# Performance work log

Measured on AMD Instinct MI355X. Metric: run time of the kernel, lower is better.

The kernel has to match this reference:

```python
import jax, jax.numpy as jnp
import numpy as np

N, E = 50000, 640000
IN, HD, OUT, NCLS = 768, 128, 128, 2
H, C = 4, 32  # heads, per-head channels (HD/H = OUT/H = 32)
NEG_SLOPE = 0.2


def _glorot(key, shape):
    fan_in, fan_out = shape[0], shape[1]
    lim = jnp.sqrt(6.0 / (fan_in + fan_out))
    return jax.random.uniform(key, shape, jnp.float32, -lim, lim)


def setup_inputs() -> dict:
    key = jax.random.key(0)
    ks = jax.random.split(key, 24)
    x = jax.random.normal(ks[0], (1, N, IN), jnp.float32)
    edge_index = jax.random.randint(ks[1], (2, E), 0, N, jnp.int64)
    d = {"x": x, "edge_index": edge_index}
    ins = [IN, HD, HD, HD]
    for i in range(4):
        d[f"Wl{i+1}"] = _glorot(ks[2 + 5 * i], (ins[i], H * C))
        d[f"Wr{i+1}"] = _glorot(ks[3 + 5 * i], (ins[i], H * C))
        d[f"att{i+1}"] = _glorot(ks[4 + 5 * i], (H, C))
        d[f"b{i+1}"] = jnp.zeros((H * C,), jnp.float32)
    d["clfW"] = _glorot(ks[22], (OUT, NCLS))
    d["clfb"] = jnp.zeros((NCLS,), jnp.float32)
    return d


def _gatv2_layer(x, Wl, Wr, att, b, src, dst):
    # x: [N, F_in] -> out: [N, H*C]. GATv2: e = a^T LeakyReLU(xl_j + xr_i)
    xl = (x @ Wl).reshape(N, H, C)
    xr = (x @ Wr).reshape(N, H, C)
    h = xl[src] + xr[dst]                                   # [E', H, C] per-edge gather
    e = jnp.einsum('ehc,hc->eh', jax.nn.leaky_relu(h, NEG_SLOPE), att)
    m = jax.ops.segment_max(e, dst, num_segments=N)          # scatter-softmax (stable)
    a = jnp.exp(e - m[dst])
    s = jax.ops.segment_sum(a, dst, num_segments=N)
    alpha = a / (s[dst] + 1e-16)
    out = jax.ops.segment_sum(alpha[..., None] * xl[src], dst, num_segments=N)
    return out.reshape(N, H * C) + b


def reference(x, edge_index, Wl1, Wr1, att1, b1, Wl2, Wr2, att2, b2,
              Wl3, Wr3, att3, b3, Wl4, Wr4, att4, b4, clfW, clfb):
    xn = x.reshape(N, IN)  # torch.squeeze
    loops = jnp.arange(N, dtype=edge_index.dtype)  # PyG add_self_loops=True
    src = jnp.concatenate([edge_index[0], loops])
    dst = jnp.concatenate([edge_index[1], loops])
    h = jax.nn.relu(_gatv2_layer(xn, Wl1, Wr1, att1, b1, src, dst))
    h = jax.nn.relu(_gatv2_layer(h, Wl2, Wr2, att2, b2, src, dst))
    h = jax.nn.relu(_gatv2_layer(h, Wl3, Wr3, att3, b3, src, dst))
    h = _gatv2_layer(h, Wl4, Wr4, att4, b4, src, dst)        # [N, OUT]
    g = jnp.mean(h, axis=0, keepdims=True)                   # unsqueeze+mean over nodes -> [1, OUT]
    return g @ clfW + clfb                                   # [1, NCLS]
```

## Files before the change

### kernel.cpp

```cpp
#include <hip/hip_runtime.h>
#include <hip/hip_bf16.h>
#include <hip/hip_fp16.h>

#define NN 50000
#define EE 640000
#define HC 128
#define NB1 196

typedef _Float16 f16x8 __attribute__((ext_vector_type(8)));
typedef _Float16 h2 __attribute__((ext_vector_type(2)));
typedef float f32x4 __attribute__((ext_vector_type(4)));
typedef unsigned short u16;

__device__ __forceinline__ u16 f2h(float f) {
    return __builtin_bit_cast(u16, (_Float16)f);
}
__device__ __forceinline__ h2 bch2(unsigned a) { return __builtin_bit_cast(h2, a); }
__device__ __forceinline__ h2 habs2(h2 a) {
    return __builtin_bit_cast(h2, __builtin_bit_cast(unsigned, a) & 0x7FFF7FFFu);
}

__device__ __forceinline__ void gload_lds16(const void* g, void* l) {
    __builtin_amdgcn_global_load_lds((const __attribute__((address_space(1))) void*)g,
                                     (__attribute__((address_space(3))) void*)l, 16, 0, 0);
}

__device__ __forceinline__ float red8(float x) {
    x += __int_as_float(__builtin_amdgcn_update_dpp(0, __float_as_int(x), 0xB1, 0xF, 0xF, true));
    x += __int_as_float(__builtin_amdgcn_update_dpp(0, __float_as_int(x), 0x4E, 0xF, 0xF, true));
    x += __int_as_float(__builtin_amdgcn_ds_swizzle(__float_as_int(x), 0x101F));
    return x;
}


__global__ void k_count(const int* __restrict__ ei, int* __restrict__ cnt) {
    int e = blockIdx.x * blockDim.x + threadIdx.x;
    if (e < EE) atomicAdd(&cnt[ei[EE + e]], 1);
}

__global__ void k_bsum(const int* __restrict__ cnt, int* __restrict__ bsum) {
    __shared__ int sd[256];
    int b = blockIdx.x, t = threadIdx.x, i = b * 256 + t;
    sd[t] = (i < NN) ? cnt[i] + 1 : 0;
    __syncthreads();
    for (int o = 128; o; o >>= 1) { if (t < o) sd[t] += sd[t + o]; __syncthreads(); }
    if (!t) bsum[b] = sd[0];
}

__global__ void k_offs(const int* __restrict__ cnt_in, const int* __restrict__ bsum,
                       int* __restrict__ offs, int* __restrict__ cursor,
                       int* __restrict__ csr) {
    __shared__ int sb[256];
    __shared__ int sd[256];
    int b = blockIdx.x, t = threadIdx.x, i = b * 256 + t;
    sb[t] = (t < NB1) ? bsum[t] : 0;
    int v = (i < NN) ? cnt_in[i] + 1 : 0;
    sd[t] = v;
    __syncthreads();
    for (int o = 1; o < 256; o <<= 1) {
        int u1 = (t >= o) ? sd[t - o] : 0;
        int u2 = (t >= o) ? sb[t - o] : 0;
        __syncthreads();
        sd[t] += u1; sb[t] += u2;
        __syncthreads();
    }
    int bex = (b > 0) ? sb[b - 1] : 0;
    if (i < NN) {
        int o = bex + sd[t] - v;
        offs[i] = o;
        csr[o] = i;
        cursor[i] = o + 1;
    }
    if (b == NB1 - 1 && t == 0) offs[NN] = sb[NB1 - 1];
}

__global__ void k_fill(const int* __restrict__ ei, int* __restrict__ cursor,
                       int* __restrict__ csr) {
    int e = blockIdx.x * blockDim.x + threadIdx.x;
    if (e < EE) {
        int s = ei[e], d = ei[EE + e];
        int pos = atomicAdd(&cursor[d], 1);
        csr[pos] = s;
    }
}


#define WT_L0 196608
#define WT_LX 32768
#define WT_TOT (WT_L0 + 3 * WT_LX)

__global__ void k_castw_all(const float* __restrict__ Wl1, const float* __restrict__ Wr1,
                            const float* __restrict__ Wl2, const float* __restrict__ Wr2,
                            const float* __restrict__ Wl3, const float* __restrict__ Wr3,
                            const float* __restrict__ Wl4, const float* __restrict__ Wr4,
                            u16* __restrict__ WtAll) {
    int gid = blockIdx.x * 256 + threadIdx.x;
    if (gid >= WT_TOT) return;
    const float *Wl, *Wr;
    int idx, K, base;
    if (gid < WT_L0) { Wl = Wl1; Wr = Wr1; idx = gid; K = 768; base = 0; }
    else {
        int r = gid - WT_L0;
        int l = r >> 15; idx = r & (WT_LX - 1); K = 128; base = WT_L0 + l * WT_LX;
        if (l == 0)      { Wl = Wl2; Wr = Wr2; }
        else if (l == 1) { Wl = Wl3; Wr = Wr3; }
        else             { Wl = Wl4; Wr = Wr4; }
    }
    int c = idx / K, k = idx - c * K;
    float v = (c < 128) ? Wl[k * 128 + c] : Wr[k * 128 + (c - 128)];
    WtAll[base + idx] = f2h(v);
}


template<int K, bool F32A>
__global__ __launch_bounds__(512, 4)
void k_gemm(const void* __restrict__ Ag, const u16* __restrict__ Wt,
            u16* __restrict__ xb) {
    __shared__ __align__(16) u16 As[128 * 64];
    __shared__ __align__(16) u16 Bs[256 * 64];
    const int tid = threadIdx.x;
    const int wv = tid >> 6, ln = tid & 63;
    const int wr = wv >> 2, wc = wv & 3;
    const int m0 = blockIdx.x * 128;
    const int lrow = ln & 15, g = ln >> 4;

    f32x4 acc[4][4] = {};

    const float* Af = (const float*)Ag;
    const u16* Ab = (const u16*)Ag;
    const int arow = tid >> 2, aq = tid & 3;
    int arg = m0 + arow; if (arg >= NN) arg = 0;
    float4 ra0, ra1, ra2, ra3;

    if constexpr (F32A) {
        const float* src = Af + (size_t)arg * K + aq * 16;
        ra0 = *(const float4*)(src);
        ra1 = *(const float4*)(src + 4);
        ra2 = *(const float4*)(src + 8);
        ra3 = *(const float4*)(src + 12);
    }

    constexpr int NSTEP = K / 64;
    for (int ks = 0; ks < NSTEP; ++ks) {
        if constexpr (F32A) {
            const int s = arow & 7;
            f16x8 v0, v1;
            v0[0] = (_Float16)ra0.x; v0[1] = (_Float16)ra0.y;
            v0[2] = (_Float16)ra0.z; v0[3] = (_Float16)ra0.w;
            v0[4] = (_Float16)ra1.x; v0[5] = (_Float16)ra1.y;
            v0[6] = (_Float16)ra1.z; v0[7] = (_Float16)ra1.w;
            v1[0] = (_Float16)ra2.x; v1[1] = (_Float16)ra2.y;
            v1[2] = (_Float16)ra2.z; v1[3] = (_Float16)ra2.w;
            v1[4] = (_Float16)ra3.x; v1[5] = (_Float16)ra3.y;
            v1[6] = (_Float16)ra3.z; v1[7] = (_Float16)ra3.w;
            *(f16x8*)&As[arow * 64 + (((aq * 2) ^ s) * 8)] = v0;
            *(f16x8*)&As[arow * 64 + (((aq * 2 + 1) ^ s) * 8)] = v1;
        } else {
            #pragma unroll
            for (int q = 0; q < 2; ++q) {
                int r8 = (wv * 2 + q) * 8;
                int row = r8 + (ln >> 3);
                int lc = (ln & 7) ^ (row & 7);
                int rg = m0 + row; if (rg >= NN) rg = 0;
                gload_lds16(Ab + (size_t)rg * K + ks * 64 + lc * 8, &As[r8 * 64]);
            }
        }
        #pragma unroll
        for (int q = 0; q < 4; ++q) {
            int r8 = (wv * 4 + q) * 8;
            int row = r8 + (ln >> 3);
            int lc = (ln & 7) ^ (row & 7);
            gload_lds16(Wt + (size_t)row * K + ks * 64 + lc * 8, &Bs[r8 * 64]);
        }
        __syncthreads();

        if constexpr (F32A) {
            if (ks + 1 < NSTEP) {
                const float* src = Af + (size_t)arg * K + (ks + 1) * 64 + aq * 16;
                ra0 = *(const float4*)(src);
                ra1 = *(const float4*)(src + 4);
                ra2 = *(const float4*)(src + 8);
                ra3 = *(const float4*)(src + 12);
            }
        }

        #pragma unroll
        for (int kk = 0; kk < 2; ++kk) {
            f16x8 af[4], bfr[4];
            #pragma unroll
            for (int f = 0; f < 4; ++f) {
                int r = wr * 64 + f * 16 + lrow;
                af[f] = *(const f16x8*)&As[r * 64 + (((kk * 4 + g) ^ (r & 7)) * 8)];
                int c = wc * 64 + f * 16 + lrow;
                bfr[f] = *(const f16x8*)&Bs[c * 64 + (((kk * 4 + g) ^ (c & 7)) * 8)];
            }
            #pragma unroll
            for (int i = 0; i < 4; ++i)
                #pragma unroll
                for (int j = 0; j < 4; ++j)
                    acc[i][j] = __builtin_amdgcn_mfma_f32_16x16x32_f16(af[i], bfr[j], acc[i][j], 0, 0, 0);
        }
        __syncthreads();
    }

    const int crow0 = m0 + wr * 64 + (g << 2);
    const int ccol0 = wc * 64 + lrow;
    #pragma unroll
    for (int i = 0; i < 4; ++i)
        #pragma unroll
        for (int rr = 0; rr < 4; ++rr) {
            int row = crow0 + i * 16 + rr;
            if (row < NN) {
                #pragma unroll
                for (int j = 0; j < 4; ++j)
                    xb[(size_t)row * 256 + ccol0 + j * 16] = f2h(acc[i][j][rr]);
            }
        }
}


__global__ __launch_bounds__(256)
void k_edge(const u16* __restrict__ xb, const float* __restrict__ att,
            const float* __restrict__ bias, const int* __restrict__ offs,
            const int* __restrict__ csr, u16* __restrict__ outb,
            float* __restrict__ outf, int relu) {
    const int wv = threadIdx.x >> 6;
    const int ln = threadIdx.x & 63;
    const int half = ln >> 5, lh = ln & 31;
    const int i = blockIdx.x * 8 + wv * 2 + half;
    const int c4 = lh * 4;

    uint2 xrw = *(const uint2*)&xb[(size_t)i * 256 + 128 + c4];
    const h2 xr01 = bch2(xrw.x), xr23 = bch2(xrw.y);
    float4 av = *(const float4*)&att[c4];
    const h2 at01 = {(_Float16)av.x, (_Float16)av.y};
    const h2 at23 = {(_Float16)av.z, (_Float16)av.w};
    const h2 C06 = {(_Float16)0.6f, (_Float16)0.6f};
    const h2 C04 = {(_Float16)0.4f, (_Float16)0.4f};

    int beg = offs[i];
    int deg = offs[i + 1] - beg;
    int degO = __shfl_xor(deg, 32);
    int degM = (deg > degO) ? deg : degO;

    float m0v = -3.0e38f, s0v = 0.f, a00 = 0.f, a01 = 0.f, a02 = 0.f, a03 = 0.f;
    float m1v = -3.0e38f, s1v = 0.f, a10 = 0.f, a11 = 0.f, a12 = 0.f, a13 = 0.f;
    float m2v = -3.0e38f, s2v = 0.f, a20 = 0.f, a21 = 0.f, a22 = 0.f, a23 = 0.f;
    float m3v = -3.0e38f, s3v = 0.f, a30 = 0.f, a31 = 0.f, a32 = 0.f, a33 = 0.f;

#define GATH(k, jj) uint2 w##k = *(const uint2*)&xb[(size_t)(jj) * 256 + c4];
#define UPD(k, M, S, A0, A1, A2, A3, ok) { \
    h2 v01 = bch2(w##k.x), v23 = bch2(w##k.y); \
    h2 u01 = v01 + xr01, u23 = v23 + xr23; \
    h2 l01 = u01 * C06 + habs2(u01) * C04; \
    h2 l23 = u23 * C06 + habs2(u23) * C04; \
    float e = __builtin_amdgcn_fdot2(l01, at01, \
              __builtin_amdgcn_fdot2(l23, at23, 0.f, false), false); \
    e = red8(e); \
    float d = e - M; \
    float tt = __expf(-fabsf(d)); \
    bool ng = (d <= 0.f) || (!(ok)); \
    float c = ng ? 1.f : tt; \
    float ww = (ok) ? (ng ? tt : 1.f) : 0.f; \
    M = ng ? M : e; \
    S = S * c + ww; \
    A0 = A0 * c + ww * (float)v01[0]; A1 = A1 * c + ww * (float)v01[1]; \
    A2 = A2 * c + ww * (float)v23[0]; A3 = A3 * c + ww * (float)v23[1]; }

    for (int base = 0; base < degM; base += 32) {
        int idxv = (base + lh < deg) ? csr[beg + base + lh] : i;
        int lim = degM - base; if (lim > 32) lim = 32;
        int myl = deg - base;
        for (int p = 0; p < lim; p += 4) {
            int j0 = __shfl(idxv, p + 0, 32);
            int j1 = __shfl(idxv, p + 1, 32);
            int j2 = __shfl(idxv, p + 2, 32);
            int j3 = __shfl(idxv, p + 3, 32);
            GATH(0, j0) GATH(1, j1) GATH(2, j2) GATH(3, j3)
            UPD(0, m0v, s0v, a00, a01, a02, a03, (p + 0 < myl))
            UPD(1, m1v, s1v, a10, a11, a12, a13, (p + 1 < myl))
            UPD(2, m2v, s2v, a20, a21, a22, a23, (p + 2 < myl))
            UPD(3, m3v, s3v, a30, a31, a32, a33, (p + 3 < myl))
        }
    }
#undef GATH
#undef UPD

    float mm = fmaxf(fmaxf(m0v, m1v), fmaxf(m2v, m3v));
    float c0 = __expf(m0v - mm), c1 = __expf(m1v - mm);
    float c2 = __expf(m2v - mm), c3 = __expf(m3v - mm);
    float s = s0v * c0 + s1v * c1 + s2v * c2 + s3v * c3 + 1e-16f;
    float inv = 1.f / s;
    float4 bv = *(const float4*)&bias[c4];
    float o0 = (a00 * c0 + a10 * c1 + a20 * c2 + a30 * c3) * inv + bv.x;
    float o1 = (a01 * c0 + a11 * c1 + a21 * c2 + a31 * c3) * inv + bv.y;
    float o2 = (a02 * c0 + a12 * c1 + a22 * c2 + a32 * c3) * inv + bv.z;
    float o3 = (a03 * c0 + a13 * c1 + a23 * c2 + a33 * c3) * inv + bv.w;
    if (relu) {
        o0 = fmaxf(o0, 0.f); o1 = fmaxf(o1, 0.f);
        o2 = fmaxf(o2, 0.f); o3 = fmaxf(o3, 0.f);
    }
    if (outb) {
        uint2 pk;
        pk.x = (unsigned)f2h(o0) | ((unsigned)f2h(o1) << 16);
        pk.y = (unsigned)f2h(o2) | ((unsigned)f2h(o3) << 16);
        *(uint2*)&outb[(size_t)i * HC + c4] = pk;
    }
    if (outf) {
        *(float4*)&outf[(size_t)i * HC + c4] = make_float4(o0, o1, o2, o3);
    }
}


__global__ __launch_bounds__(256)
void k_colsum(const float* __restrict__ h, float* __restrict__ gsum) {
    __shared__ float4 sd[8][32];
    int t = threadIdx.x;
    int c4 = t & 31, rl = t >> 5;
    float sx = 0.f, sy = 0.f, sz = 0.f, sw = 0.f;
    for (int r = blockIdx.x * 8 + rl; r < NN; r += 8 * gridDim.x) {
        float4 v = *(const float4*)&h[(size_t)r * HC + c4 * 4];
        sx += v.x; sy += v.y; sz += v.z; sw += v.w;
    }
    sd[rl][c4] = make_float4(sx, sy, sz, sw);
    __syncthreads();
    if (rl == 0) {
        float4 a = sd[0][c4];
        #pragma unroll
        for (int q = 1; q < 8; ++q) {
            float4 b = sd[q][c4];
            a.x += b.x; a.y += b.y; a.z += b.z; a.w += b.w;
        }
        atomicAdd(&gsum[c4 * 4 + 0], a.x);
        atomicAdd(&gsum[c4 * 4 + 1], a.y);
        atomicAdd(&gsum[c4 * 4 + 2], a.z);
        atomicAdd(&gsum[c4 * 4 + 3], a.w);
    }
}

__global__ void k_clf(const float* __restrict__ gsum, const float* __restrict__ W,
                      const float* __restrict__ bcls, float* __restrict__ out) {
    __shared__ float v[HC];
    int t = threadIdx.x;
    v[t] = gsum[t] * (1.f / (float)NN);
    __syncthreads();
    if (t < 2) {
        float r = 0.f;
        for (int k = 0; k < HC; ++k) r += v[k] * W[k * 2 + t];
        out[t] = r + bcls[t];
    }
}


extern "C" void kernel_launch(void* const* d_in, const int* in_sizes, int n_in,
                              void* d_out, int out_size, void* d_ws, size_t ws_size,
                              hipStream_t stream) {
    const float* x = (const float*)d_in[0];
    const int* ei = (const int*)d_in[1];
    const float *Wl[4], *Wr[4], *att[4], *bia[4];
    for (int l = 0; l < 4; ++l) {
        Wl[l] = (const float*)d_in[2 + 4 * l];
        Wr[l] = (const float*)d_in[3 + 4 * l];
        att[l] = (const float*)d_in[4 + 4 * l];
        bia[l] = (const float*)d_in[5 + 4 * l];
    }
    const float* clfW = (const float*)d_in[18];
    const float* clfb = (const float*)d_in[19];
    float* outp = (float*)d_out;

    char* w = (char*)d_ws;
    size_t o = 0;
    auto alloc = [&](size_t bytes) {
        char* p = w + o;
        o = (o + bytes + 255) & ~(size_t)255;
        return p;
    };
    int* cnt    = (int*)alloc((size_t)NN * 4);
    float* gsum = (float*)alloc(HC * 4);
    size_t zspan = o;
    int* offs  = (int*)alloc((size_t)(NN + 1) * 4);
    int* csr   = (int*)alloc((size_t)(EE + NN) * 4);
    int* bsum  = (int*)alloc((size_t)NB1 * 4);
    u16* WtAll = (u16*)alloc((size_t)WT_TOT * 2);
    u16* xb    = (u16*)alloc((size_t)NN * 256 * 2);
    u16* hb0   = (u16*)alloc((size_t)NN * HC * 2);
    u16* hb1   = (u16*)alloc((size_t)NN * HC * 2);
    float* hfin = (float*)alloc((size_t)NN * HC * 4);

    hipMemsetAsync(cnt, 0, zspan, stream);
    k_count<<<(EE + 255) / 256, 256, 0, stream>>>(ei, cnt);
    k_bsum<<<NB1, 256, 0, stream>>>(cnt, bsum);
    k_offs<<<NB1, 256, 0, stream>>>(cnt, bsum, offs, cnt, csr);
    k_fill<<<(EE + 255) / 256, 256, 0, stream>>>(ei, cnt, csr);
    k_castw_all<<<(WT_TOT + 255) / 256, 256, 0, stream>>>(
        Wl[0], Wr[0], Wl[1], Wr[1], Wl[2], Wr[2], Wl[3], Wr[3], WtAll);

    const int GB = (NN + 127) / 128;
    const u16* Wt_l[4] = {WtAll, WtAll + WT_L0, WtAll + WT_L0 + WT_LX,
                          WtAll + WT_L0 + 2 * WT_LX};
    const u16* hb_in = nullptr;
    u16* hbb[2] = {hb0, hb1};
    for (int l = 0; l < 4; ++l) {
        if (l == 0) k_gemm<768, true ><<<GB, 512, 0, stream>>>((const void*)x, Wt_l[0], xb);
        else        k_gemm<128, false><<<GB, 512, 0, stream>>>((const void*)hb_in, Wt_l[l], xb);
        u16* ob = (l < 3) ? hbb[l & 1] : nullptr;
        float* of = (l == 3) ? hfin : nullptr;
        k_edge<<<NN / 8, 256, 0, stream>>>(xb, att[l], bia[l], offs, csr, ob, of,
                                           (l < 3) ? 1 : 0);
        hb_in = ob;
    }

    k_colsum<<<504, 256, 0, stream>>>(hfin, gsum);
    k_clf<<<1, 128, 0, stream>>>(gsum, clfW, clfb, outp);
}
```

Baseline: 364.8 us.

## Specialize K=128 GEMM with single-stage LDS and fuse final column sum into edge kernel

Splits the templated GEMM into a dedicated layer-0 kernel and a new K=128 kernel. The new kernel loads the whole 128x128 A tile into LDS in one pass and keeps B fragments in registers read straight from global memory. The last edge-aggregation layer now reduces its outputs per block into a small partial-sum buffer through shared-memory atomics, so the full N x 128 fp32 output is never written or re-read. The extra __syncthreads and LDS atomics add some cost to the last edge layer, and register use rises in the new GEMM.

```diff
diff --git a/kernel.cpp b/kernel.cpp
--- a/kernel.cpp
+++ b/kernel.cpp
@@ -6,6 +6,7 @@
 #define EE 640000
 #define HC 128
 #define NB1 196
+#define NEB 6250
 
 typedef _Float16 f16x8 __attribute__((ext_vector_type(8)));
 typedef _Float16 h2 __attribute__((ext_vector_type(2)));
@@ -112,10 +113,10 @@
 }
 
 
-template<int K, bool F32A>
 __global__ __launch_bounds__(512, 4)
-void k_gemm(const void* __restrict__ Ag, const u16* __restrict__ Wt,
-            u16* __restrict__ xb) {
+void k_gemm0(const float* __restrict__ Af, const u16* __restrict__ Wt,
+             u16* __restrict__ xb) {
+    constexpr int K = 768;
     __shared__ __align__(16) u16 As[128 * 64];
     __shared__ __align__(16) u16 Bs[256 * 64];
     const int tid = threadIdx.x;
@@ -126,13 +127,11 @@
 
     f32x4 acc[4][4] = {};
 
-    const float* Af = (const float*)Ag;
-    const u16* Ab = (const u16*)Ag;
     const int arow = tid >> 2, aq = tid & 3;
     int arg = m0 + arow; if (arg >= NN) arg = 0;
     float4 ra0, ra1, ra2, ra3;
 
-    if constexpr (F32A) {
+    {
         const float* src = Af + (size_t)arg * K + aq * 16;
         ra0 = *(const float4*)(src);
         ra1 = *(const float4*)(src + 4);
@@ -142,7 +141,7 @@
 
     constexpr int NSTEP = K / 64;
     for (int ks = 0; ks < NSTEP; ++ks) {
-        if constexpr (F32A) {
+        {
             const int s = arow & 7;
             f16x8 v0, v1;
             v0[0] = (_Float16)ra0.x; v0[1] = (_Float16)ra0.y;
@@ -155,15 +154,6 @@
             v1[6] = (_Float16)ra3.z; v1[7] = (_Float16)ra3.w;
             *(f16x8*)&As[arow * 64 + (((aq * 2) ^ s) * 8)] = v0;
             *(f16x8*)&As[arow * 64 + (((aq * 2 + 1) ^ s) * 8)] = v1;
-        } else {
-            #pragma unroll
-            for (int q = 0; q < 2; ++q) {
-                int r8 = (wv * 2 + q) * 8;
-                int row = r8 + (ln >> 3);
-                int lc = (ln & 7) ^ (row & 7);
-                int rg = m0 + row; if (rg >= NN) rg = 0;
-                gload_lds16(Ab + (size_t)rg * K + ks * 64 + lc * 8, &As[r8 * 64]);
-            }
         }
         #pragma unroll
         for (int q = 0; q < 4; ++q) {
@@ -174,14 +164,12 @@
         }
         __syncthreads();
 
-        if constexpr (F32A) {
-            if (ks + 1 < NSTEP) {
-                const float* src = Af + (size_t)arg * K + (ks + 1) * 64 + aq * 16;
-                ra0 = *(const float4*)(src);
-                ra1 = *(const float4*)(src + 4);
-                ra2 = *(const float4*)(src + 8);
-                ra3 = *(const float4*)(src + 12);
-            }
+        if (ks + 1 < NSTEP) {
+            const float* src = Af + (size_t)arg * K + (ks + 1) * 64 + aq * 16;
+            ra0 = *(const float4*)(src);
+            ra1 = *(const float4*)(src + 4);
+            ra2 = *(const float4*)(src + 8);
+            ra3 = *(const float4*)(src + 12);
         }
 
         #pragma unroll
@@ -219,16 +207,80 @@
 }
 
 
+__global__ __launch_bounds__(512)
+void k_gemm_s(const u16* __restrict__ A, const u16* __restrict__ Wt,
+              u16* __restrict__ xb) {
+    __shared__ __align__(16) u16 As[128 * 128];
+    const int tid = threadIdx.x;
+    const int wv = tid >> 6, ln = tid & 63;
+    const int wr = wv >> 2, wc = wv & 3;
+    const int m0 = blockIdx.x * 128;
+    const int lrow = ln & 15, g = ln >> 4;
+
+    #pragma unroll
+    for (int q = 0; q < 4; ++q) {
+        int seg = wv * 4 + q;
+        int row = seg * 4 + g;
+        int lc = lrow ^ (row & 15);
+        int rg = m0 + row; if (rg >= NN) rg = 0;
+        gload_lds16(A + (size_t)rg * 128 + lc * 8, &As[seg * 512]);
+    }
+    f16x8 bfr[4][4];
+    #pragma unroll
+    for (int j = 0; j < 4; ++j) {
+        int col = wc * 64 + j * 16 + lrow;
+        #pragma unroll
+        for (int kk = 0; kk < 4; ++kk)
+            bfr[j][kk] = *(const f16x8*)&Wt[(size_t)col * 128 + kk * 32 + g * 8];
+    }
+    __syncthreads();
+
+    f32x4 acc[4][4] = {};
+    #pragma unroll
+    for (int kk = 0; kk < 4; ++kk) {
+        f16x8 af[4];
+        #pragma unroll
+        for (int f = 0; f < 4; ++f) {
+            int r = wr * 64 + f * 16 + lrow;
+            int pc = (kk * 4 + g) ^ (r & 15);
+            af[f] = *(const f16x8*)&As[r * 128 + pc * 8];
+        }
+        #pragma unroll
+        for (int i = 0; i < 4; ++i)
+            #pragma unroll
+            for (int j = 0; j < 4; ++j)
+                acc[i][j] = __builtin_amdgcn_mfma_f32_16x16x32_f16(af[i], bfr[j][kk], acc[i][j], 0, 0, 0);
+    }
+
+    const int crow0 = m0 + wr * 64 + (g << 2);
+    const int ccol0 = wc * 64 + lrow;
+    #pragma unroll
+    for (int i = 0; i < 4; ++i)
+        #pragma unroll
+        for (int rr = 0; rr < 4; ++rr) {
+            int row = crow0 + i * 16 + rr;
+            if (row < NN) {
+                #pragma unroll
+                for (int j = 0; j < 4; ++j)
+                    xb[(size_t)row * 256 + ccol0 + j * 16] = f2h(acc[i][j][rr]);
+            }
+        }
+}
+
+
 __global__ __launch_bounds__(256)
 void k_edge(const u16* __restrict__ xb, const float* __restrict__ att,
             const float* __restrict__ bias, const int* __restrict__ offs,
             const int* __restrict__ csr, u16* __restrict__ outb,
-            float* __restrict__ outf, int relu) {
+            float* __restrict__ part, int relu) {
+    __shared__ float ps[HC];
     const int wv = threadIdx.x >> 6;
     const int ln = threadIdx.x & 63;
     const int half = ln >> 5, lh = ln & 31;
     const int i = blockIdx.x * 8 + wv * 2 + half;
     const int c4 = lh * 4;
+
+    if (part && threadIdx.x < HC) ps[threadIdx.x] = 0.f;
 
     uint2 xrw = *(const uint2*)&xb[(size_t)i * 256 + 128 + c4];
     const h2 xr01 = bch2(xrw.x), xr23 = bch2(xrw.y);
@@ -306,19 +358,26 @@
         pk.y = (unsigned)f2h(o2) | ((unsigned)f2h(o3) << 16);
         *(uint2*)&outb[(size_t)i * HC + c4] = pk;
     }
-    if (outf) {
-        *(float4*)&outf[(size_t)i * HC + c4] = make_float4(o0, o1, o2, o3);
+    if (part) {
+        __syncthreads();
+        atomicAdd(&ps[c4 + 0], o0);
+        atomicAdd(&ps[c4 + 1], o1);
+        atomicAdd(&ps[c4 + 2], o2);
+        atomicAdd(&ps[c4 + 3], o3);
+        __syncthreads();
+        if (threadIdx.x < HC)
+            part[(size_t)blockIdx.x * HC + threadIdx.x] = ps[threadIdx.x];
     }
 }
 
 
 __global__ __launch_bounds__(256)
-void k_colsum(const float* __restrict__ h, float* __restrict__ gsum) {
+void k_colsum(const float* __restrict__ h, float* __restrict__ gsum, int nr) {
     __shared__ float4 sd[8][32];
     int t = threadIdx.x;
     int c4 = t & 31, rl = t >> 5;
     float sx = 0.f, sy = 0.f, sz = 0.f, sw = 0.f;
-    for (int r = blockIdx.x * 8 + rl; r < NN; r += 8 * gridDim.x) {
+    for (int r = blockIdx.x * 8 + rl; r < nr; r += 8 * gridDim.x) {
         float4 v = *(const float4*)&h[(size_t)r * HC + c4 * 4];
         sx += v.x; sy += v.y; sz += v.z; sw += v.w;
     }
@@ -385,7 +444,7 @@
     u16* xb    = (u16*)alloc((size_t)NN * 256 * 2);
     u16* hb0   = (u16*)alloc((size_t)NN * HC * 2);
     u16* hb1   = (u16*)alloc((size_t)NN * HC * 2);
-    float* hfin = (float*)alloc((size_t)NN * HC * 4);
+    float* part = (float*)alloc((size_t)NEB * HC * 4);
 
     hipMemsetAsync(cnt, 0, zspan, stream);
     k_count<<<(EE + 255) / 256, 256, 0, stream>>>(ei, cnt);
@@ -401,15 +460,15 @@
     const u16* hb_in = nullptr;
     u16* hbb[2] = {hb0, hb1};
     for (int l = 0; l < 4; ++l) {
-        if (l == 0) k_gemm<768, true ><<<GB, 512, 0, stream>>>((const void*)x, Wt_l[0], xb);
-        else        k_gemm<128, false><<<GB, 512, 0, stream>>>((const void*)hb_in, Wt_l[l], xb);
+        if (l == 0) k_gemm0<<<GB, 512, 0, stream>>>(x, Wt_l[0], xb);
+        else        k_gemm_s<<<GB, 512, 0, stream>>>(hb_in, Wt_l[l], xb);
         u16* ob = (l < 3) ? hbb[l & 1] : nullptr;
-        float* of = (l == 3) ? hfin : nullptr;
-        k_edge<<<NN / 8, 256, 0, stream>>>(xb, att[l], bia[l], offs, csr, ob, of,
-                                           (l < 3) ? 1 : 0);
+        float* pp = (l == 3) ? part : nullptr;
+        k_edge<<<NEB, 256, 0, stream>>>(xb, att[l], bia[l], offs, csr, ob, pp,
+                                        (l < 3) ? 1 : 0);
         hb_in = ob;
     }
 
-    k_colsum<<<504, 256, 0, stream>>>(hfin, gsum);
+    k_colsum<<<64, 256, 0, stream>>>(part, gsum, NEB);
     k_clf<<<1, 128, 0, stream>>>(gsum, clfW, clfb, outp);
 }
```

Result: no change. 372.0 us (+2.0%).
